# Kernel tuning notes

Hardware: AMD Instinct MI355X
Metric: run time of the kernel (lower is better)

The kernel has to match this reference:

```python
import jax, jax.numpy as jnp
import numpy as np

KERNEL_MUL = 2.0
KERNEL_NUM = 5


def _mmd(source, target):
    n_s = source.shape[0]
    total = jnp.concatenate([source, target], axis=0)  # (2N, D)
    n = total.shape[0]
    # pairwise squared L2 via a^2 + b^2 - 2ab (avoids (2N,2N,D) intermediate)
    sq = jnp.sum(total * total, axis=1)  # (2N,)
    L2 = sq[:, None] + sq[None, :] - 2.0 * (total @ total.T)  # (2N, 2N)
    # torch uses L2_distance.data for bandwidth -> stop_gradient
    bandwidth = jax.lax.stop_gradient(jnp.sum(L2)) / (n * n - n)
    bandwidth = bandwidth / (KERNEL_MUL ** (KERNEL_NUM // 2))
    # multi-bandwidth RBF sum
    kernels = jnp.zeros_like(L2)
    for i in range(KERNEL_NUM):
        kernels = kernels + jnp.exp(-L2 / (bandwidth * KERNEL_MUL ** i))
    XX = kernels[:n_s, :n_s]
    YY = kernels[n_s:, n_s:]
    XY = kernels[:n_s, n_s:]
    YX = kernels[n_s:, :n_s]
    return jnp.mean(XX) + jnp.mean(YY) - jnp.mean(XY) - jnp.mean(YX)


def setup_inputs() -> dict:
    key = jax.random.key(0)
    k1, k2 = jax.random.split(key)
    source = jax.random.normal(k1, (4096, 256), dtype=jnp.float32)
    target = jax.random.normal(k2, (4096, 256), dtype=jnp.float32) + 0.5
    return {"source": source, "target": target}


def reference(source, target):
    return _mmd(source, target)
```

## Files before the change

kernel.cpp:

```cpp
#include <hip/hip_runtime.h>

typedef short bf16x8 __attribute__((ext_vector_type(8)));
typedef float f32x4 __attribute__((ext_vector_type(4)));

#define KDIM 256
#define BT 128
#define BK 64
#define SBLK 256

__device__ __forceinline__ unsigned short f2bf(float f) {
  unsigned u = __float_as_uint(f);
  unsigned r = (u + 0x7fffu + ((u >> 16) & 1u)) >> 16;
  return (unsigned short)r;
}
__device__ __forceinline__ float bf2f(unsigned short b) {
  return __uint_as_float(((unsigned)b) << 16);
}

__device__ __forceinline__ void async_cp16(const void* g, void* l) {
  __builtin_amdgcn_global_load_lds(
      (const __attribute__((address_space(1))) unsigned int*)g,
      (__attribute__((address_space(3))) unsigned int*)l, 16, 0, 0);
}

__device__ __forceinline__ float2 pk_add(float2 a, float2 b) {
  return make_float2(a.x + b.x, a.y + b.y);
}
__device__ __forceinline__ float2 pk_mul(float2 a, float2 b) {
  return make_float2(a.x * b.x, a.y * b.y);
}
__device__ __forceinline__ float2 pk_fma(float2 a, float2 b, float2 c) {
  return make_float2(__builtin_fmaf(a.x, b.x, c.x),
                     __builtin_fmaf(a.y, b.y, c.y));
}

__global__ __launch_bounds__(256) void mmd_stage(
    const float* __restrict__ src, const float* __restrict__ tgt, int ns,
    unsigned short* __restrict__ Tbf, float* __restrict__ sq,
    float* __restrict__ pscol, float* __restrict__ psums) {
  __shared__ float sp[256];
  __shared__ float rw[4];
  int t = threadIdx.x;
  int lane = t & 63, wave = t >> 6;
  sp[t] = 0.f;
  __syncthreads();
  int sub = t & 31;
  int rsel = t >> 5;
  float colacc[8];
#pragma unroll
  for (int j = 0; j < 8; ++j) colacc[j] = 0.f;
  float tsq = 0.f;
#pragma unroll
  for (int it = 0; it < 4; ++it) {
    int r = blockIdx.x * 32 + it * 8 + rsel;
    const float* rp = (r < ns) ? (src + (size_t)r * KDIM)
                               : (tgt + (size_t)(r - ns) * KDIM);
    float4 v0 = *(const float4*)(rp + sub * 8);
    float4 v1 = *(const float4*)(rp + sub * 8 + 4);
    float vals[8] = {v0.x, v0.y, v0.z, v0.w, v1.x, v1.y, v1.z, v1.w};
    unsigned pk[4];
    float ssp = 0.f;
#pragma unroll
    for (int j = 0; j < 4; ++j) {
      unsigned short b0 = f2bf(vals[2 * j]);
      unsigned short b1 = f2bf(vals[2 * j + 1]);
      float x0 = bf2f(b0), x1 = bf2f(b1);
      pk[j] = (unsigned)b0 | ((unsigned)b1 << 16);
      ssp += x0 * x0 + x1 * x1;
      colacc[2 * j] += x0;
      colacc[2 * j + 1] += x1;
    }
    *(uint4*)(Tbf + (size_t)r * KDIM + sub * 8) =
        make_uint4(pk[0], pk[1], pk[2], pk[3]);
    tsq += ssp;
    float ss = ssp;
#pragma unroll
    for (int off = 16; off; off >>= 1) ss += __shfl_down(ss, off, 32);
    if (sub == 0) sq[r] = ss;
  }
#pragma unroll
  for (int j = 0; j < 8; ++j) atomicAdd(&sp[sub * 8 + j], colacc[j]);
#pragma unroll
  for (int off = 32; off; off >>= 1) tsq += __shfl_down(tsq, off, 64);
  if (lane == 0) rw[wave] = tsq;
  __syncthreads();
  pscol[(size_t)blockIdx.x * 256 + t] = sp[t];
  if (t == 0) psums[blockIdx.x] = rw[0] + rw[1] + rw[2] + rw[3];
}

__global__ __launch_bounds__(256) void mmd_prep2(
    const float* __restrict__ pscol, const float* __restrict__ psums,
    float* __restrict__ coef, float* __restrict__ out, int n) {
  __shared__ float redP[4], redS[4];
  int t = threadIdx.x;
  int lane = t & 63, wave = t >> 6;
  float cs = 0.f;
#pragma unroll 8
  for (int b = 0; b < SBLK; ++b) cs += pscol[(size_t)b * 256 + t];
  float p = cs * cs;
  float s = psums[t];
#pragma unroll
  for (int off = 32; off; off >>= 1) {
    p += __shfl_down(p, off, 64);
    s += __shfl_down(s, off, 64);
  }
  if (lane == 0) { redP[wave] = p; redS[wave] = s; }
  __syncthreads();
  if (t == 0) {
    double ssq = (double)(redP[0] + redP[1] + redP[2] + redP[3]);
    double S = (double)(redS[0] + redS[1] + redS[2] + redS[3]);
    double nn = (double)n;
    double sumL2 = 2.0 * nn * S - 2.0 * ssq;
    double bw = sumL2 / (nn * nn - nn) / 4.0;
    coef[0] = (float)(-1.4426950408889634 / (16.0 * bw));
    out[0] = 0.f;
  }
}

__global__ __launch_bounds__(256) void mmd_main(
    const unsigned short* __restrict__ Tbf, const float* __restrict__ sq,
    const float* __restrict__ coef, float* __restrict__ out, int halfTiles,
    float inv) {
  __shared__ short As[BT * BK];
  __shared__ short Bs[BT * BK];
  __shared__ float sqa[BT];
  __shared__ float sqb[BT];
  __shared__ float red[4];

  int id = blockIdx.x;
  int bi = (int)((sqrtf(8.f * (float)id + 1.f) - 1.f) * 0.5f);
  while ((bi + 1) * (bi + 2) / 2 <= id) ++bi;
  while (bi * (bi + 1) / 2 > id) --bi;
  int bj = id - bi * (bi + 1) / 2;
  int rowBase = bi * BT, colBase = bj * BT;

  int t = threadIdx.x;
  int lane = t & 63, wave = t >> 6;

  if (t < 128) sqa[t] = sq[rowBase + t];
  else sqb[t - 128] = sq[colBase + (t - 128)];

  f32x4 acc[4][4];
#pragma unroll
  for (int a = 0; a < 4; ++a)
#pragma unroll
    for (int b = 0; b < 4; ++b) {
      f32x4 z = {0.f, 0.f, 0.f, 0.f};
      acc[a][b] = z;
    }

  int wrow = (wave >> 1) * 64, wcol = (wave & 1) * 64;
  int lrow = lane >> 3;
  int kgsw = (lane & 7) ^ lrow;
  int frow = lane & 15;
  int kq = lane >> 4;

  for (int c = 0; c < 4; ++c) {
    int k0 = c * BK;
#pragma unroll
    for (int j = 0; j < 4; ++j) {
      int R0 = j * 32 + wave * 8;
      int ldsoff = (j * 256 + wave * 64) * 8;
      async_cp16(Tbf + (size_t)(rowBase + R0 + lrow) * KDIM + k0 + kgsw * 8,
                 &As[ldsoff]);
      async_cp16(Tbf + (size_t)(colBase + R0 + lrow) * KDIM + k0 + kgsw * 8,
                 &Bs[ldsoff]);
    }
    __syncthreads();
#pragma unroll
    for (int ks = 0; ks < 2; ++ks) {
      bf16x8 af[4], bfv[4];
#pragma unroll
      for (int mt = 0; mt < 4; ++mt) {
        int r = wrow + mt * 16 + frow;
        int pg = (ks * 4 + kq) ^ (r & 7);
        af[mt] = *(const bf16x8*)&As[r * BK + pg * 8];
      }
#pragma unroll
      for (int nt = 0; nt < 4; ++nt) {
        int r = wcol + nt * 16 + frow;
        int pg = (ks * 4 + kq) ^ (r & 7);
        bfv[nt] = *(const bf16x8*)&Bs[r * BK + pg * 8];
      }
#pragma unroll
      for (int mt = 0; mt < 4; ++mt)
#pragma unroll
        for (int nt = 0; nt < 4; ++nt)
          acc[mt][nt] = __builtin_amdgcn_mfma_f32_16x16x32_bf16(
              af[mt], bfv[nt], acc[mt][nt], 0, 0, 0);
    }
    __syncthreads();
  }

  float c4 = coef[0];
  float m2c4 = -2.f * c4;
  float2 m2v = make_float2(m2c4, m2c4);
  int ccol = lane & 15;
  int rb = (lane >> 4) * 4;
  float ra[16];
#pragma unroll
  for (int mt = 0; mt < 4; ++mt)
#pragma unroll
    for (int rg = 0; rg < 4; ++rg)
      ra[mt * 4 + rg] = sqa[wrow + mt * 16 + rb + rg] * c4;
  float cbv[4];
#pragma unroll
  for (int nt = 0; nt < 4; ++nt) cbv[nt] = sqb[wcol + nt * 16 + ccol] * c4;

  float2 lsum2 = make_float2(0.f, 0.f);
#pragma unroll
  for (int mt = 0; mt < 4; ++mt) {
#pragma unroll
    for (int nt = 0; nt < 4; ++nt) {
      float cb = cbv[nt];
#pragma unroll
      for (int rp = 0; rp < 4; rp += 2) {
        float2 g = make_float2(acc[mt][nt][rp], acc[mt][nt][rp + 1]);
        float2 sab =
            make_float2(ra[mt * 4 + rp] + cb, ra[mt * 4 + rp + 1] + cb);
        float2 u = pk_fma(g, m2v, sab);
        float2 e = make_float2(__builtin_amdgcn_exp2f(u.x),
                               __builtin_amdgcn_exp2f(u.y));
        float2 e2 = pk_mul(e, e);
        float2 e4 = pk_mul(e2, e2);
        float2 e8 = pk_mul(e4, e4);
        float2 s = pk_add(e, e2);
        s = pk_add(s, e4);
        s = pk_add(s, e8);
        s = pk_fma(e8, e8, s);
        lsum2 = pk_add(lsum2, s);
      }
    }
  }
  float lsum = lsum2.x + lsum2.y;
#pragma unroll
  for (int off = 32; off; off >>= 1) lsum += __shfl_down(lsum, off, 64);
  if (lane == 0) red[wave] = lsum;
  __syncthreads();
  if (t == 0) {
    float w = ((bi < halfTiles) == (bj < halfTiles)) ? 1.f : -1.f;
    float f = (bi == bj) ? 1.f : 2.f;
    atomicAdd(out, w * f * inv * (red[0] + red[1] + red[2] + red[3]));
  }
}

extern "C" void kernel_launch(void* const* d_in, const int* in_sizes, int n_in,
                              void* d_out, int out_size, void* d_ws,
                              size_t ws_size, hipStream_t stream) {
  const float* src = (const float*)d_in[0];
  const float* tgt = (const float*)d_in[1];
  int ns = in_sizes[0] / KDIM;
  int ntr = in_sizes[1] / KDIM;
  int n = ns + ntr;

  char* ws = (char*)d_ws;
  unsigned short* Tbf = (unsigned short*)ws;
  size_t off = (size_t)n * KDIM * sizeof(unsigned short);
  float* sq = (float*)(ws + off);    off += (size_t)n * 4;
  float* pscol = (float*)(ws + off); off += (size_t)SBLK * 256 * 4;
  float* psums = (float*)(ws + off); off += SBLK * 4;
  float* coef = (float*)(ws + off);

  float* out = (float*)d_out;
  int nb = n / BT;
  int nTiles = nb * (nb + 1) / 2;

  mmd_stage<<<SBLK, 256, 0, stream>>>(src, tgt, ns, Tbf, sq, pscol, psums);
  mmd_prep2<<<1, 256, 0, stream>>>(pscol, psums, coef, out, n);
  mmd_main<<<nTiles, 256, 0, stream>>>(Tbf, sq, coef, out, ns / BT,
                                       1.f / ((float)ns * (float)ns));
}
```

Baseline: 114.4 us.

## Load MFMA operands directly from global memory instead of staging through LDS

Drops the LDS tiles and async global-to-LDS copies in the main Gram kernel. Each wave now reads its bf16x8 MFMA fragments straight from global memory (relying on L1/L2 caching) over a fully unrolled K loop. This removes the LDS round trip and the per-chunk barriers. The cost is redundant global/cache traffic, since fragments shared between waves are re-fetched, and more exposed load latency.

```diff
diff --git a/kernel.cpp b/kernel.cpp
--- a/kernel.cpp
+++ b/kernel.cpp
@@ -5,7 +5,6 @@
 
 #define KDIM 256
 #define BT 128
-#define BK 64
 #define SBLK 256
 
 __device__ __forceinline__ unsigned short f2bf(float f) {
@@ -15,12 +14,6 @@
 }
 __device__ __forceinline__ float bf2f(unsigned short b) {
   return __uint_as_float(((unsigned)b) << 16);
-}
-
-__device__ __forceinline__ void async_cp16(const void* g, void* l) {
-  __builtin_amdgcn_global_load_lds(
-      (const __attribute__((address_space(1))) unsigned int*)g,
-      (__attribute__((address_space(3))) unsigned int*)l, 16, 0, 0);
 }
 
 __device__ __forceinline__ float2 pk_add(float2 a, float2 b) {
@@ -121,8 +114,6 @@
     const unsigned short* __restrict__ Tbf, const float* __restrict__ sq,
     const float* __restrict__ coef, float* __restrict__ out, int halfTiles,
     float inv) {
-  __shared__ short As[BT * BK];
-  __shared__ short Bs[BT * BK];
   __shared__ float sqa[BT];
   __shared__ float sqb[BT];
   __shared__ float red[4];
@@ -139,6 +130,20 @@
 
   if (t < 128) sqa[t] = sq[rowBase + t];
   else sqb[t - 128] = sq[colBase + (t - 128)];
+  __syncthreads();
+
+  int wrow = (wave >> 1) * 64, wcol = (wave & 1) * 64;
+  int frow = lane & 15;
+  int kq = lane >> 4;
+
+  const unsigned short* aB[4];
+  const unsigned short* bB[4];
+#pragma unroll
+  for (int mt = 0; mt < 4; ++mt)
+    aB[mt] = Tbf + (size_t)(rowBase + wrow + mt * 16 + frow) * KDIM + kq * 8;
+#pragma unroll
+  for (int nt = 0; nt < 4; ++nt)
+    bB[nt] = Tbf + (size_t)(colBase + wcol + nt * 16 + frow) * KDIM + kq * 8;
 
   f32x4 acc[4][4];
 #pragma unroll
@@ -149,47 +154,21 @@
       acc[a][b] = z;
     }
 
-  int wrow = (wave >> 1) * 64, wcol = (wave & 1) * 64;
-  int lrow = lane >> 3;
-  int kgsw = (lane & 7) ^ lrow;
-  int frow = lane & 15;
-  int kq = lane >> 4;
-
-  for (int c = 0; c < 4; ++c) {
-    int k0 = c * BK;
-#pragma unroll
-    for (int j = 0; j < 4; ++j) {
-      int R0 = j * 32 + wave * 8;
-      int ldsoff = (j * 256 + wave * 64) * 8;
-      async_cp16(Tbf + (size_t)(rowBase + R0 + lrow) * KDIM + k0 + kgsw * 8,
-                 &As[ldsoff]);
-      async_cp16(Tbf + (size_t)(colBase + R0 + lrow) * KDIM + k0 + kgsw * 8,
-                 &Bs[ldsoff]);
-    }
-    __syncthreads();
-#pragma unroll
-    for (int ks = 0; ks < 2; ++ks) {
-      bf16x8 af[4], bfv[4];
-#pragma unroll
-      for (int mt = 0; mt < 4; ++mt) {
-        int r = wrow + mt * 16 + frow;
-        int pg = (ks * 4 + kq) ^ (r & 7);
-        af[mt] = *(const bf16x8*)&As[r * BK + pg * 8];
-      }
-#pragma unroll
-      for (int nt = 0; nt < 4; ++nt) {
-        int r = wcol + nt * 16 + frow;
-        int pg = (ks * 4 + kq) ^ (r & 7);
-        bfv[nt] = *(const bf16x8*)&Bs[r * BK + pg * 8];
-      }
-#pragma unroll
-      for (int mt = 0; mt < 4; ++mt)
-#pragma unroll
-        for (int nt = 0; nt < 4; ++nt)
-          acc[mt][nt] = __builtin_amdgcn_mfma_f32_16x16x32_bf16(
-              af[mt], bfv[nt], acc[mt][nt], 0, 0, 0);
-    }
-    __syncthreads();
+#pragma unroll
+  for (int ks = 0; ks < 8; ++ks) {
+    bf16x8 af[4], bfv[4];
+#pragma unroll
+    for (int mt = 0; mt < 4; ++mt)
+      af[mt] = *(const bf16x8*)(aB[mt] + ks * 32);
+#pragma unroll
+    for (int nt = 0; nt < 4; ++nt)
+      bfv[nt] = *(const bf16x8*)(bB[nt] + ks * 32);
+#pragma unroll
+    for (int mt = 0; mt < 4; ++mt)
+#pragma unroll
+      for (int nt = 0; nt < 4; ++nt)
+        acc[mt][nt] = __builtin_amdgcn_mfma_f32_16x16x32_bf16(
+            af[mt], bfv[nt], acc[mt][nt], 0, 0, 0);
   }
 
   float c4 = coef[0];
```

Result: slower. 145.3 us (+27.0%).
